# Performance work log

Hardware: AMD Instinct MI355X
Metric: run time of the kernel (lower is better)

The kernel has to match this reference:

```python
import jax, jax.numpy as jnp
import numpy as np
from jax import lax

WINDOW_SIZE = 11
CHANNEL = 3
SIGMA = 1.5


def _gaussian_window(ws=WINDOW_SIZE, ch=CHANNEL, sigma=SIGMA):
    x = np.arange(ws, dtype=np.float64)
    g = np.exp(-((x - ws // 2) ** 2) / (2.0 * sigma ** 2))
    g = g / g.sum()
    w2 = np.outer(g, g).astype(np.float32)  # [ws, ws]
    w = np.broadcast_to(w2, (ch, 1, ws, ws)).copy()  # depthwise OIHW, groups=ch
    return jnp.asarray(w)


def _depthwise_conv(x, w):
    pad = WINDOW_SIZE // 2
    return lax.conv_general_dilated(
        x, w, window_strides=(1, 1), padding=[(pad, pad), (pad, pad)],
        dimension_numbers=('NCHW', 'OIHW', 'NCHW'),
        feature_group_count=CHANNEL)


def setup_inputs() -> dict:
    key = jax.random.key(0)
    k1, k2 = jax.random.split(key)
    shape = (16, 3, 512, 512)
    img1 = jax.random.uniform(k1, shape, dtype=jnp.float32)
    img2 = jax.random.uniform(k2, shape, dtype=jnp.float32)
    return {"img1": img1, "img2": img2}


def reference(img1, img2):
    window = _gaussian_window()
    img1 = jnp.clip(jnp.nan_to_num(img1, nan=0.0), 0.0, 1.0)
    img2 = jnp.clip(jnp.nan_to_num(img2, nan=0.0), 0.0, 1.0)

    C1 = 0.01 ** 2 + 1e-06
    C2 = 0.03 ** 2 + 1e-06

    mu1 = _depthwise_conv(img1, window)
    mu2 = _depthwise_conv(img2, window)
    mu1_sq = mu1 * mu1
    mu2_sq = mu2 * mu2
    mu1_mu2 = mu1 * mu2

    sigma1_sq = _depthwise_conv(img1 * img1, window) - mu1_sq
    sigma2_sq = _depthwise_conv(img2 * img2, window) - mu2_sq
    sigma12 = _depthwise_conv(img1 * img2, window) - mu1_mu2

    sigma1_sq = jnp.clip(sigma1_sq, 1e-06, 1e6)
    sigma2_sq = jnp.clip(sigma2_sq, 1e-06, 1e6)

    ssim_map = (2.0 * mu1_mu2 + C1) * (2.0 * sigma12 + C2) / (
        (mu1_sq + mu2_sq + C1) * (sigma1_sq + sigma2_sq + C2))
    ssim_map = jnp.nan_to_num(ssim_map, nan=0.0)

    return 1.0 - jnp.mean(ssim_map)  # size_average=True -> scalar
```

## Files before the change

kernel.cpp:

```cpp
#include <hip/hip_runtime.h>


typedef float v2f __attribute__((ext_vector_type(2)));

#define IMG    512
#define SCOLS  128
#define SROWS  32
#define NSTEPS 42
#define BUFW   288
#define NPIX   (16.0f * 3.0f * 512.0f * 512.0f)

__device__ __forceinline__ float clamp01(float x) {
    return fminf(fmaxf(x, 0.0f), 1.0f);
}

__device__ __forceinline__ float ssim_px(v2f mu, v2f e, float e12, float C1, float C2) {
    v2f musq = mu * mu;
    float mu12 = mu.x * mu.y;
    v2f sig = e - musq;
    v2f lo = {1e-6f, 1e-6f};
    v2f hi = {1e6f, 1e6f};
    sig = __builtin_elementwise_max(sig, lo);
    sig = __builtin_elementwise_min(sig, hi);
    float s12 = e12 - mu12;
    float num = fmaf(2.f, mu12, C1) * fmaf(2.f, s12, C2);
    float den = (musq.x + musq.y + C1) * (sig.x + sig.y + C2);
    return num * __builtin_amdgcn_rcpf(den);
}

__global__ __launch_bounds__(64, 2)
void ssim_stream_kernel(const float* __restrict__ imgA,
                        const float* __restrict__ imgB,
                        float* __restrict__ accum)
{
    constexpr float GW[11] = {
        0.00102838f, 0.00759880f, 0.03600077f, 0.10936070f, 0.21300554f,
        0.26601173f,
        0.21300554f, 0.10936070f, 0.03600077f, 0.00759880f, 0.00102838f
    };
    const float C1 = 1.01e-4f;
    const float C2 = 9.01e-4f;

    __shared__ float sbuf[2][BUFW];

    const int lane = threadIdx.x;
    const int C0 = blockIdx.x * SCOLS;
    const int R0 = blockIdx.y * SROWS;
    const size_t pOff = (size_t)blockIdx.z * (size_t)(IMG * IMG);

    const int t0   = lane;
    const int q0   = (t0 < 36) ? t0 : (t0 - 36);
    const float* sp0 = ((t0 < 36) ? imgA : imgB) + pOff;
    const int col0 = C0 - 8 + 4 * q0;
    const bool okc0 = (col0 >= 0) && (col0 <= IMG - 4);
    const int wd0  = 8 * q0 + ((t0 < 36) ? 0 : 1);
    const bool has1 = (lane < 8);
    const int q1   = 28 + lane;
    const int col1 = C0 - 8 + 4 * q1;
    const bool okc1 = (col1 >= 0) && (col1 <= IMG - 4);
    const int wd1  = 8 * q1 + 1;
    const float* sp1 = imgB + pOff;

    v2f rA[11][2], rB[11][2];
    float rC[11][2];
#pragma unroll
    for (int i = 0; i < 11; ++i) {
        rA[i][0] = 0; rA[i][1] = 0;
        rB[i][0] = 0; rB[i][1] = 0;
        rC[i][0] = 0; rC[i][1] = 0;
    }

    float lsum = 0.f;

    float4 p0 = make_float4(0,0,0,0), p1 = make_float4(0,0,0,0);
    {
        int ir = R0 - 5;
        bool okr = (unsigned)ir < (unsigned)IMG;
        if (okr && okc0) p0 = *(const float4*)(sp0 + (size_t)ir * IMG + col0);
        if (has1 && okr && okc1) p1 = *(const float4*)(sp1 + (size_t)ir * IMG + col1);
    }

#pragma unroll 1
    for (int ch = 0; ch < 4; ++ch) {
#pragma unroll
        for (int u = 0; u < 11; ++u) {
            const int s = ch * 11 + u;
            if (s < NSTEPS) {
                const int par = s & 1;

                {
                    float* d0 = &sbuf[par][wd0];
                    d0[0] = clamp01(p0.x); d0[2] = clamp01(p0.y);
                    d0[4] = clamp01(p0.z); d0[6] = clamp01(p0.w);
                    if (has1) {
                        float* d1 = &sbuf[par][wd1];
                        d1[0] = clamp01(p1.x); d1[2] = clamp01(p1.y);
                        d1[4] = clamp01(p1.z); d1[6] = clamp01(p1.w);
                    }
                }

                if (s + 1 < NSTEPS) {
                    int ir = R0 - 5 + s + 1;
                    bool okr = (unsigned)ir < (unsigned)IMG;
                    p0 = make_float4(0,0,0,0);
                    p1 = make_float4(0,0,0,0);
                    if (okr && okc0) p0 = *(const float4*)(sp0 + (size_t)ir * IMG + col0);
                    if (has1 && okr && okc1) p1 = *(const float4*)(sp1 + (size_t)ir * IMG + col1);
                }

                {
                    const v2f* wp = (const v2f*)(&sbuf[par][0]) + (2 * lane + 3);
                    v2f w[12];
#pragma unroll
                    for (int p = 0; p < 12; ++p) w[p] = wp[p];

                    v2f hA0 = 0, hB0 = 0, hA1 = 0, hB1 = 0;
                    float hC0 = 0, hC1 = 0;
#pragma unroll
                    for (int j = 0; j < 11; ++j) {
                        const float gj = GW[j];
                        v2f w0 = w[j], w1 = w[j + 1];
                        v2f g0 = gj * w0;
                        v2f g1 = gj * w1;
                        hA0 += g0;
                        hA1 += g1;
                        hB0 += g0 * w0;
                        hB1 += g1 * w1;
                        hC0 = fmaf(g0.x, w0.y, hC0);
                        hC1 = fmaf(g1.x, w1.y, hC1);
                    }
                    rA[u][0] = hA0; rA[u][1] = hA1;
                    rB[u][0] = hB0; rB[u][1] = hB1;
                    rC[u][0] = hC0; rC[u][1] = hC1;
                }

                if (s >= 10) {
                    v2f vA0 = 0, vB0 = 0, vA1 = 0, vB1 = 0;
                    float vC0 = 0, vC1 = 0;
#pragma unroll
                    for (int i = 0; i < 11; ++i) {
                        const int sl = (u + 1 + i) % 11;
                        const float gi = GW[i];
                        vA0 += gi * rA[sl][0]; vA1 += gi * rA[sl][1];
                        vB0 += gi * rB[sl][0]; vB1 += gi * rB[sl][1];
                        vC0 = fmaf(gi, rC[sl][0], vC0);
                        vC1 = fmaf(gi, rC[sl][1], vC1);
                    }
                    lsum += ssim_px(vA0, vB0, vC0, C1, C2);
                    lsum += ssim_px(vA1, vB1, vC1, C1, C2);
                }
            }
        }
    }

#pragma unroll
    for (int off = 32; off >= 1; off >>= 1)
        lsum += __shfl_down(lsum, off, 64);
    if (lane == 0) atomicAdd(accum, lsum);
}

__global__ void ssim_finalize_kernel(const float* __restrict__ accum,
                                     float* __restrict__ out) {
    out[0] = 1.0f - accum[0] * (1.0f / NPIX);
}

extern "C" void kernel_launch(void* const* d_in, const int* in_sizes, int n_in,
                              void* d_out, int out_size, void* d_ws, size_t ws_size,
                              hipStream_t stream) {
    const float* img1 = (const float*)d_in[0];
    const float* img2 = (const float*)d_in[1];
    float* out = (float*)d_out;
    float* ws  = (float*)d_ws;

    hipMemsetAsync(ws, 0, sizeof(float), stream);

    dim3 grid(IMG / SCOLS, IMG / SROWS, 48);
    ssim_stream_kernel<<<grid, 64, 0, stream>>>(img1, img2, ws);
    ssim_finalize_kernel<<<1, 1, 0, stream>>>(ws, out);
}
```

Baseline: 205.6 us.

## Restructure SSIM kernel to one column per lane with two waves per block

Each lane now computes a single output column instead of two. The strip height is halved to 16 rows and blocks carry two independent 64-wide waves, which gives many more waves and lower register pressure for better latency hiding. Staging now interleaves A/B pixels with vectorized 16-byte LDS stores, and global loads are prefetched two rows ahead through a 12-slot register ring. The cost is more halo work: each block reads 26 input rows to produce 16 output rows, and the horizontal pass is recomputed over a larger fraction of overlapping rows and columns.

```diff
diff --git a/kernel.cpp b/kernel.cpp
--- a/kernel.cpp
+++ b/kernel.cpp
@@ -2,19 +2,22 @@
 
 
 typedef float v2f __attribute__((ext_vector_type(2)));
+typedef float v4f __attribute__((ext_vector_type(4)));
 
 #define IMG    512
-#define SCOLS  128
-#define SROWS  32
-#define NSTEPS 42
-#define BUFW   288
+#define WCOLS  64
+#define SROWS  16
+#define NSTEPS 26
+#define BUFW   160
 #define NPIX   (16.0f * 3.0f * 512.0f * 512.0f)
 
 __device__ __forceinline__ float clamp01(float x) {
     return fminf(fmaxf(x, 0.0f), 1.0f);
 }
 
-__device__ __forceinline__ float ssim_px(v2f mu, v2f e, float e12, float C1, float C2) {
+__device__ __forceinline__ float ssim_px(v2f mu, v2f e, float e12) {
+    const float C1 = 1.01e-4f;
+    const float C2 = 9.01e-4f;
     v2f musq = mu * mu;
     float mu12 = mu.x * mu.y;
     v2f sig = e - musq;
@@ -28,7 +31,7 @@
     return num * __builtin_amdgcn_rcpf(den);
 }
 
-__global__ __launch_bounds__(64, 2)
+__global__ __launch_bounds__(128, 4)
 void ssim_stream_kernel(const float* __restrict__ imgA,
                         const float* __restrict__ imgB,
                         float* __restrict__ accum)
@@ -38,120 +41,110 @@
         0.26601173f,
         0.21300554f, 0.10936070f, 0.03600077f, 0.00759880f, 0.00102838f
     };
-    const float C1 = 1.01e-4f;
-    const float C2 = 9.01e-4f;
 
-    __shared__ float sbuf[2][BUFW];
+    __shared__ __attribute__((aligned(16))) float sb0[2][BUFW];
+    __shared__ __attribute__((aligned(16))) float sb1[2][BUFW];
 
-    const int lane = threadIdx.x;
-    const int C0 = blockIdx.x * SCOLS;
+    const int tid  = threadIdx.x;
+    const int wv   = tid >> 6;
+    const int lane = tid & 63;
+    float* b0 = sb0[wv];
+    float* b1 = sb1[wv];
+
+    const int C0 = blockIdx.x * (2 * WCOLS) + wv * WCOLS;
     const int R0 = blockIdx.y * SROWS;
     const size_t pOff = (size_t)blockIdx.z * (size_t)(IMG * IMG);
+    const float* pA = imgA + pOff;
+    const float* pB = imgB + pOff;
 
-    const int t0   = lane;
-    const int q0   = (t0 < 36) ? t0 : (t0 - 36);
-    const float* sp0 = ((t0 < 36) ? imgA : imgB) + pOff;
-    const int col0 = C0 - 8 + 4 * q0;
-    const bool okc0 = (col0 >= 0) && (col0 <= IMG - 4);
-    const int wd0  = 8 * q0 + ((t0 < 36) ? 0 : 1);
-    const bool has1 = (lane < 8);
-    const int q1   = 28 + lane;
-    const int col1 = C0 - 8 + 4 * q1;
-    const bool okc1 = (col1 >= 0) && (col1 <= IMG - 4);
-    const int wd1  = 8 * q1 + 1;
-    const float* sp1 = imgB + pOff;
+    const bool stg  = lane < 20;
+    const int col0  = C0 - 8 + 4 * lane;
+    const bool okc  = stg && (col0 >= 0) && (col0 <= IMG - 4);
+    const int wbase = 8 * lane;
 
-    v2f rA[11][2], rB[11][2];
-    float rC[11][2];
+    v2f rA[12], rB[12];
+    float rC[12];
 #pragma unroll
-    for (int i = 0; i < 11; ++i) {
-        rA[i][0] = 0; rA[i][1] = 0;
-        rB[i][0] = 0; rB[i][1] = 0;
-        rC[i][0] = 0; rC[i][1] = 0;
-    }
+    for (int i = 0; i < 12; ++i) { rA[i] = 0; rB[i] = 0; rC[i] = 0; }
+
+    float4 na = make_float4(0, 0, 0, 0), nb = na;
+
+    auto fetch = [&](int s, float4& qa, float4& qb) {
+        qa = make_float4(0, 0, 0, 0);
+        qb = make_float4(0, 0, 0, 0);
+        const int ir = R0 - 5 + s;
+        if (okc && (unsigned)ir < (unsigned)IMG && s < NSTEPS) {
+            qa = *(const float4*)(pA + (size_t)ir * IMG + col0);
+            qb = *(const float4*)(pB + (size_t)ir * IMG + col0);
+        }
+    };
+    auto stage = [&](float* dst, const float4& qa, const float4& qb) {
+        if (stg) {
+            v4f w0 = {clamp01(qa.x), clamp01(qb.x), clamp01(qa.y), clamp01(qb.y)};
+            v4f w1 = {clamp01(qa.z), clamp01(qb.z), clamp01(qa.w), clamp01(qb.w)};
+            *(v4f*)(dst + wbase)     = w0;
+            *(v4f*)(dst + wbase + 4) = w1;
+        }
+    };
 
     float lsum = 0.f;
 
-    float4 p0 = make_float4(0,0,0,0), p1 = make_float4(0,0,0,0);
+    auto body = [&](int s, int u, bool dovert) {
+        float* src = (u & 1) ? b1 : b0;
+        float* dst = (u & 1) ? b0 : b1;
+
+        v2f w[11];
+        const v2f* wp = (const v2f*)src + (lane + 3);
+#pragma unroll
+        for (int j = 0; j < 11; ++j) w[j] = wp[j];
+
+        stage(dst, na, nb);
+
+        fetch(s + 2, na, nb);
+
+        v2f hA = 0, hB = 0;
+        float hC = 0;
+#pragma unroll
+        for (int j = 0; j < 11; ++j) {
+            v2f wj = w[j];
+            v2f g  = GW[j] * wj;
+            hA += g;
+            hB += g * wj;
+            hC  = fmaf(g.x, wj.y, hC);
+        }
+        rA[u] = hA; rB[u] = hB; rC[u] = hC;
+
+        if (dovert) {
+            v2f vA = 0, vB = 0;
+            float vC = 0;
+#pragma unroll
+            for (int i = 0; i < 11; ++i) {
+                const int sl = (u + 2 + i) % 12;
+                const float gi = GW[i];
+                vA += gi * rA[sl];
+                vB += gi * rB[sl];
+                vC  = fmaf(gi, rC[sl], vC);
+            }
+            lsum += ssim_px(vA, vB, vC);
+        }
+    };
+
     {
-        int ir = R0 - 5;
-        bool okr = (unsigned)ir < (unsigned)IMG;
-        if (okr && okc0) p0 = *(const float4*)(sp0 + (size_t)ir * IMG + col0);
-        if (has1 && okr && okc1) p1 = *(const float4*)(sp1 + (size_t)ir * IMG + col1);
+        float4 qa, qb;
+        fetch(0, qa, qb);
+        stage(b0, qa, qb);
+        fetch(1, na, nb);
     }
 
 #pragma unroll 1
-    for (int ch = 0; ch < 4; ++ch) {
+    for (int ch = 0; ch < 24; ch += 12) {
 #pragma unroll
-        for (int u = 0; u < 11; ++u) {
-            const int s = ch * 11 + u;
-            if (s < NSTEPS) {
-                const int par = s & 1;
-
-                {
-                    float* d0 = &sbuf[par][wd0];
-                    d0[0] = clamp01(p0.x); d0[2] = clamp01(p0.y);
-                    d0[4] = clamp01(p0.z); d0[6] = clamp01(p0.w);
-                    if (has1) {
-                        float* d1 = &sbuf[par][wd1];
-                        d1[0] = clamp01(p1.x); d1[2] = clamp01(p1.y);
-                        d1[4] = clamp01(p1.z); d1[6] = clamp01(p1.w);
-                    }
-                }
-
-                if (s + 1 < NSTEPS) {
-                    int ir = R0 - 5 + s + 1;
-                    bool okr = (unsigned)ir < (unsigned)IMG;
-                    p0 = make_float4(0,0,0,0);
-                    p1 = make_float4(0,0,0,0);
-                    if (okr && okc0) p0 = *(const float4*)(sp0 + (size_t)ir * IMG + col0);
-                    if (has1 && okr && okc1) p1 = *(const float4*)(sp1 + (size_t)ir * IMG + col1);
-                }
-
-                {
-                    const v2f* wp = (const v2f*)(&sbuf[par][0]) + (2 * lane + 3);
-                    v2f w[12];
-#pragma unroll
-                    for (int p = 0; p < 12; ++p) w[p] = wp[p];
-
-                    v2f hA0 = 0, hB0 = 0, hA1 = 0, hB1 = 0;
-                    float hC0 = 0, hC1 = 0;
-#pragma unroll
-                    for (int j = 0; j < 11; ++j) {
-                        const float gj = GW[j];
-                        v2f w0 = w[j], w1 = w[j + 1];
-                        v2f g0 = gj * w0;
-                        v2f g1 = gj * w1;
-                        hA0 += g0;
-                        hA1 += g1;
-                        hB0 += g0 * w0;
-                        hB1 += g1 * w1;
-                        hC0 = fmaf(g0.x, w0.y, hC0);
-                        hC1 = fmaf(g1.x, w1.y, hC1);
-                    }
-                    rA[u][0] = hA0; rA[u][1] = hA1;
-                    rB[u][0] = hB0; rB[u][1] = hB1;
-                    rC[u][0] = hC0; rC[u][1] = hC1;
-                }
-
-                if (s >= 10) {
-                    v2f vA0 = 0, vB0 = 0, vA1 = 0, vB1 = 0;
-                    float vC0 = 0, vC1 = 0;
-#pragma unroll
-                    for (int i = 0; i < 11; ++i) {
-                        const int sl = (u + 1 + i) % 11;
-                        const float gi = GW[i];
-                        vA0 += gi * rA[sl][0]; vA1 += gi * rA[sl][1];
-                        vB0 += gi * rB[sl][0]; vB1 += gi * rB[sl][1];
-                        vC0 = fmaf(gi, rC[sl][0], vC0);
-                        vC1 = fmaf(gi, rC[sl][1], vC1);
-                    }
-                    lsum += ssim_px(vA0, vB0, vC0, C1, C2);
-                    lsum += ssim_px(vA1, vB1, vC1, C1, C2);
-                }
-            }
+        for (int u = 0; u < 12; ++u) {
+            body(ch + u, u, (ch + u) >= 10);
         }
     }
+    body(24, 0, true);
+    body(25, 1, true);
 
 #pragma unroll
     for (int off = 32; off >= 1; off >>= 1)
@@ -174,7 +167,7 @@
 
     hipMemsetAsync(ws, 0, sizeof(float), stream);
 
-    dim3 grid(IMG / SCOLS, IMG / SROWS, 48);
-    ssim_stream_kernel<<<grid, 64, 0, stream>>>(img1, img2, ws);
+    dim3 grid(IMG / (2 * WCOLS), IMG / SROWS, 48);
+    ssim_stream_kernel<<<grid, 128, 0, stream>>>(img1, img2, ws);
     ssim_finalize_kernel<<<1, 1, 0, stream>>>(ws, out);
 }
```

After: 282.5 us. 1.37x slower.
